# Kernel tuning notes

Hardware: AMD Instinct MI355X
Metric: run time of the kernel (lower is better)

Reference implementation:

```python
import jax, jax.numpy as jnp
import numpy as np

C = 64
K = 16
DEPTH = 4            # int(sqrt(K))
N_NODES = K - 1      # 15 internal nodes per subspace tree
D = 512              # input feature dim, D // C = 8 per subspace
M = 512              # output dim (LUT rows)
N = 16384            # number of input rows


def _make_selection_matrix(C, depth=DEPTH):
    # row i within a subspace selects the transformed dim used at tree level of node i
    lvl = [0, 1, 1, 2, 2, 2, 2, 3, 3, 3, 3, 3, 3, 3, 3]
    S = np.zeros((C * N_NODES, C * depth), np.float32)
    for c in range(C):
        for i in range(N_NODES):
            S[c * N_NODES + i, c * depth + lvl[i]] = 1.0
    return S


def _make_bit_matrix(C, K=K):
    # per-subspace (K, K-1) matrix: leaf k gets +/-1 on the 4 nodes along its root-to-leaf path
    Bm = np.zeros((K, N_NODES), np.float32)
    for k in range(K):
        node = 0
        for l in range(DEPTH):
            bit = (k >> (DEPTH - 1 - l)) & 1
            Bm[k, node] = 1.0 if bit else -1.0
            node = 2 * node + 1 + bit  # children of node i are 2i+1 (left) and 2i+2 (right)
    Bfull = np.zeros((C * K, C * N_NODES), np.float32)
    for c in range(C):
        Bfull[c * K:(c + 1) * K, c * N_NODES:(c + 1) * N_NODES] = Bm
    return Bfull


def setup_inputs() -> dict:
    key = jax.random.key(0)
    k1, k2, k3, k4 = jax.random.split(key, 4)
    I = jax.random.normal(k1, (N, D), dtype=jnp.float32)
    A = jax.random.normal(k2, (C, D // C, DEPTH), dtype=jnp.float32) * (1.0 / np.sqrt(D // C))
    T = jax.random.normal(k3, (C * N_NODES,), dtype=jnp.float32) * 0.1
    L = jax.random.normal(k4, (M, C, K), dtype=jnp.float32)
    S = jnp.asarray(_make_selection_matrix(C))
    B = jnp.asarray(_make_bit_matrix(C))
    return {"I": I, "A": A, "T": T, "L": L, "S": S, "B": B}


def reference(I, A, T, L, S, B):
    C_, sub, depth = A.shape
    Kq = L.shape[-1]
    n = I.shape[0]
    # block-diagonal per-subspace projection: (n, D) -> (n, C*depth)
    Ir = I.T.reshape(C_, sub, n)                      # (C, sub, n)
    xt = jnp.einsum('csn,csd->cdn', Ir, A)            # (C, depth, n)
    xt = xt.reshape(C_ * depth, n)                    # (C*depth, n)
    # tree encoding: per-node activations, tanh relaxation, leaf scores
    h = S @ xt - T[:, None]                           # (C*15, n)
    b = (B @ jnp.tanh(h)).reshape(C_, Kq, n)          # (C, K, n)
    # straight-through hard one-hot encoding with softmax backward
    E_soft = jax.nn.softmax(b, axis=1)
    E_hard = jax.nn.one_hot(jnp.argmax(b, axis=1), Kq, axis=1, dtype=b.dtype)
    E = E_hard + E_soft - jax.lax.stop_gradient(E_soft)  # (C, K, n)
    # LUT decode: out[n, m] = sum_c L[m, c, enc(n, c)]
    out = jnp.einsum('mck,ckn->nm', L, E)
    return out
```

## Files before the change

kernel.cpp:

```cpp
#include <hip/hip_runtime.h>
#include <hip/hip_fp16.h>
#include <math.h>

#define CC 64
#define KK 16
#define NNODES 15
#define DD 512
#define MM 512
#define NN 16384

typedef _Float16 half8 __attribute__((ext_vector_type(8)));
typedef float f32x4 __attribute__((ext_vector_type(4)));
typedef unsigned long long u64;

__device__ __forceinline__ float xla_tanhf(float x) {
    const float kMax = 7.90531110763549805f;
    bool tiny = fabsf(x) < 0.0004f;
    float xc = fminf(fmaxf(x, -kMax), kMax);
    float x2 = __fmul_rn(xc, xc);
    float p = __fmaf_rn(x2, -2.76076847742355e-16f, 2.00018790482477e-13f);
    p = __fmaf_rn(x2, p, -8.60467152213735e-11f);
    p = __fmaf_rn(x2, p, 5.12229709037114e-08f);
    p = __fmaf_rn(x2, p, 1.48572235717979e-05f);
    p = __fmaf_rn(x2, p, 6.37261928875436e-04f);
    p = __fmaf_rn(x2, p, 4.89352455891786e-03f);
    p = __fmul_rn(xc, p);
    float q = __fmaf_rn(x2, 1.19825839466702e-06f, 1.18534705686654e-04f);
    q = __fmaf_rn(x2, q, 2.26843463243900e-03f);
    q = __fmaf_rn(x2, q, 4.89352518554385e-03f);
    return tiny ? x : __fdiv_rn(p, q);
}

__global__ __launch_bounds__(256) void pack_bfrag(const float* __restrict__ L,
                                                  uint4* __restrict__ Bpk) {
    const int t    = blockIdx.x * 256 + threadIdx.x;
    const int lane = t & 63;
    const int mtg  = (t >> 6) & 31;
    const int ks   = t >> 11;
    const int kbase = ks * 32 + ((lane >> 4) << 3);
    const int c     = kbase >> 4;
    const int slot0 = kbase & 15;
    const int m     = (mtg << 4) + (lane & 15);

    const float* src = L + ((size_t)m * CC + c) * KK + slot0;
    float4 v0 = ((const float4*)src)[0];
    float4 v1 = ((const float4*)src)[1];
    union { half8 h; uint4 u; } pk;
    pk.h[0] = (_Float16)v0.x; pk.h[1] = (_Float16)v0.y;
    pk.h[2] = (_Float16)v0.z; pk.h[3] = (_Float16)v0.w;
    pk.h[4] = (_Float16)v1.x; pk.h[5] = (_Float16)v1.y;
    pk.h[6] = (_Float16)v1.z; pk.h[7] = (_Float16)v1.w;
    Bpk[t] = pk.u;
}

__global__ __launch_bounds__(256, 2) void fused_mfma(const float* __restrict__ I,
                                                     const float* __restrict__ A,
                                                     const float* __restrict__ T,
                                                     const uint4* __restrict__ Bpk,
                                                     float* __restrict__ out) {
    __shared__ float sA[32 * 64];
    __shared__ float sT[CC * NNODES];
    __shared__ unsigned char sCodes[CC * 68];

    const int tid = threadIdx.x;
    for (int i = tid; i < CC * 32; i += 256) sA[(i & 31) * 64 + (i >> 5)] = A[i];
    for (int i = tid; i < CC * NNODES; i += 256) sT[i] = T[i];
    __syncthreads();

    const int w    = tid >> 6;
    const int lane = tid & 63;
    const int n0 = (blockIdx.x >> 1) * 64;
    const int m0 = (blockIdx.x & 1) * 256 + w * 64;

    {
        const int c = lane;
        const int lvl[NNODES] = {0, 1, 1, 2, 2, 2, 2, 3, 3, 3, 3, 3, 3, 3, 3};
#pragma unroll 2
        for (int rr = 0; rr < 16; ++rr) {
            const int rl = (rr << 2) + w;
            const float* Ij = I + (size_t)(n0 + rl) * DD + c * 8;
            float4 v0 = ((const float4*)Ij)[0];
            float4 v1 = ((const float4*)Ij)[1];
            float iv[8] = {v0.x, v0.y, v0.z, v0.w, v1.x, v1.y, v1.z, v1.w};

            float t[4] = {0.f, 0.f, 0.f, 0.f};
#pragma unroll
            for (int s = 0; s < 8; ++s) {
                float v = iv[s];
#pragma unroll
                for (int d = 0; d < 4; ++d)
                    t[d] = __fmaf_rn(v, sA[((s << 2) + d) * 64 + c], t[d]);
            }

            float th[NNODES];
#pragma unroll
            for (int i = 0; i < NNODES; ++i) {
                float h = __fsub_rn(t[lvl[i]], sT[c * NNODES + i]);
                th[i] = xla_tanhf(h);
            }

            int best = 0;
            float bestv = -3.0e38f;
#pragma unroll
            for (int k = 0; k < KK; ++k) {
                int node = 0;
                float s = 0.f;
#pragma unroll
                for (int l = 0; l < 4; ++l) {
                    int bit = (k >> (3 - l)) & 1;
                    s = __fadd_rn(s, bit ? th[node] : -th[node]);
                    node = 2 * node + 1 + bit;
                }
                if (s > bestv) { bestv = s; best = k; }
            }
            sCodes[c * 68 + rl] = (unsigned char)best;
        }
    }
    __syncthreads();

    const int r15  = lane & 15;
    const int sb   = ((lane >> 4) & 1) << 3;
    const int chi  = lane >> 5;
    const int mtg0 = m0 >> 4;

    f32x4 acc[4][4];
#pragma unroll
    for (int nt = 0; nt < 4; ++nt)
#pragma unroll
        for (int mt = 0; mt < 4; ++mt)
            acc[nt][mt] = (f32x4){0.f, 0.f, 0.f, 0.f};

    const uint4* Bp = Bpk + (size_t)mtg0 * 64 + lane;

    uint4 bA[4], bB[4];
#pragma unroll
    for (int mt = 0; mt < 4; ++mt) bA[mt] = Bp[mt * 64];

    for (int ks = 0; ks < 32; ks += 2) {
#pragma unroll
        for (int mt = 0; mt < 4; ++mt) bB[mt] = Bp[((ks + 1) * 32 + mt) * 64];

        half8 a0[4];
        {
            const int c0 = (ks << 1) + chi;
#pragma unroll
            for (int nt = 0; nt < 4; ++nt) {
                unsigned ud = (unsigned)((int)sCodes[c0 * 68 + (nt << 4) + r15] - sb);
                unsigned ud2 = ud - 4u;
                u64 lo = (ud  < 4u) ? (0x3C00ull << ((ud  & 3u) << 4)) : 0ull;
                u64 hi = (ud2 < 4u) ? (0x3C00ull << ((ud2 & 3u) << 4)) : 0ull;
                union { u64 q[2]; half8 h; } uu; uu.q[0] = lo; uu.q[1] = hi;
                a0[nt] = uu.h;
            }
        }
#pragma unroll
        for (int nt = 0; nt < 4; ++nt)
#pragma unroll
            for (int mt = 0; mt < 4; ++mt) {
                union { uint4 u; half8 h; } bb; bb.u = bA[mt];
                acc[nt][mt] = __builtin_amdgcn_mfma_f32_16x16x32_f16(a0[nt], bb.h, acc[nt][mt], 0, 0, 0);
            }

        if (ks + 2 < 32) {
#pragma unroll
            for (int mt = 0; mt < 4; ++mt) bA[mt] = Bp[((ks + 2) * 32 + mt) * 64];
        }

        half8 a1[4];
        {
            const int c1 = ((ks + 1) << 1) + chi;
#pragma unroll
            for (int nt = 0; nt < 4; ++nt) {
                unsigned ud = (unsigned)((int)sCodes[c1 * 68 + (nt << 4) + r15] - sb);
                unsigned ud2 = ud - 4u;
                u64 lo = (ud  < 4u) ? (0x3C00ull << ((ud  & 3u) << 4)) : 0ull;
                u64 hi = (ud2 < 4u) ? (0x3C00ull << ((ud2 & 3u) << 4)) : 0ull;
                union { u64 q[2]; half8 h; } uu; uu.q[0] = lo; uu.q[1] = hi;
                a1[nt] = uu.h;
            }
        }
#pragma unroll
        for (int nt = 0; nt < 4; ++nt)
#pragma unroll
            for (int mt = 0; mt < 4; ++mt) {
                union { uint4 u; half8 h; } bb; bb.u = bB[mt];
                acc[nt][mt] = __builtin_amdgcn_mfma_f32_16x16x32_f16(a1[nt], bb.h, acc[nt][mt], 0, 0, 0);
            }
    }

    const int rbase = (lane >> 4) << 2;
#pragma unroll
    for (int nt = 0; nt < 4; ++nt) {
#pragma unroll
        for (int r = 0; r < 4; ++r) {
            float* o = out + (size_t)(n0 + (nt << 4) + rbase + r) * MM + m0 + r15;
#pragma unroll
            for (int mt = 0; mt < 4; ++mt)
                o[mt << 4] = acc[nt][mt][r];
        }
    }
}

extern "C" void kernel_launch(void* const* d_in, const int* in_sizes, int n_in,
                              void* d_out, int out_size, void* d_ws, size_t ws_size,
                              hipStream_t stream) {
    const float* I = (const float*)d_in[0];
    const float* A = (const float*)d_in[1];
    const float* T = (const float*)d_in[2];
    const float* L = (const float*)d_in[3];

    uint4* Bpk = (uint4*)d_ws;
    float* out = (float*)d_out;

    hipLaunchKernelGGL(pack_bfrag, dim3(256), dim3(256), 0, stream, L, Bpk);
    hipLaunchKernelGGL(fused_mfma, dim3(NN / 16 / 4 * 2), dim3(256), 0, stream, I, A, T, Bpk, out);
}
```

Before: 130.2 us.

## Use 512-thread blocks with narrower per-wave M tiles and packed code words

Doubles the block to 8 waves, with each wave covering 32 output columns instead of 64. This halves the accumulator registers per wave and splits the encoding work over 8 waves instead of 4. Codes are stored in shared memory as packed 4-byte words, one per (row, subspace) group, so each MFMA step needs one LDS read per k-step instead of four byte reads. B-fragment and code loads are software-prefetched one iteration ahead. The goal is higher occupancy and latency hiding, at the cost of a smaller N×M tile per wave, which may raise the global B-fragment traffic per FLOP.

```diff
diff --git a/kernel.cpp b/kernel.cpp
--- a/kernel.cpp
+++ b/kernel.cpp
@@ -53,31 +53,31 @@
     Bpk[t] = pk.u;
 }
 
-__global__ __launch_bounds__(256, 2) void fused_mfma(const float* __restrict__ I,
+__global__ __launch_bounds__(512, 4) void fused_mfma(const float* __restrict__ I,
                                                      const float* __restrict__ A,
                                                      const float* __restrict__ T,
                                                      const uint4* __restrict__ Bpk,
                                                      float* __restrict__ out) {
     __shared__ float sA[32 * 64];
     __shared__ float sT[CC * NNODES];
-    __shared__ unsigned char sCodes[CC * 68];
+    __shared__ unsigned sCodes[16 * 68];
 
     const int tid = threadIdx.x;
-    for (int i = tid; i < CC * 32; i += 256) sA[(i & 31) * 64 + (i >> 5)] = A[i];
-    for (int i = tid; i < CC * NNODES; i += 256) sT[i] = T[i];
+    for (int i = tid; i < CC * 32; i += 512) sA[(i & 31) * 64 + (i >> 5)] = A[i];
+    for (int i = tid; i < CC * NNODES; i += 512) sT[i] = T[i];
     __syncthreads();
 
     const int w    = tid >> 6;
     const int lane = tid & 63;
     const int n0 = (blockIdx.x >> 1) * 64;
-    const int m0 = (blockIdx.x & 1) * 256 + w * 64;
+    const int m0 = (blockIdx.x & 1) * 256 + w * 32;
 
     {
         const int c = lane;
         const int lvl[NNODES] = {0, 1, 1, 2, 2, 2, 2, 3, 3, 3, 3, 3, 3, 3, 3};
 #pragma unroll 2
-        for (int rr = 0; rr < 16; ++rr) {
-            const int rl = (rr << 2) + w;
+        for (int rr = 0; rr < 8; ++rr) {
+            const int rl = (rr << 3) + w;
             const float* Ij = I + (size_t)(n0 + rl) * DD + c * 8;
             float4 v0 = ((const float4*)Ij)[0];
             float4 v1 = ((const float4*)Ij)[1];
@@ -113,7 +113,7 @@
                 }
                 if (s > bestv) { bestv = s; best = k; }
             }
-            sCodes[c * 68 + rl] = (unsigned char)best;
+            ((unsigned char*)&sCodes[(rl & 15) * 68 + c])[rl >> 4] = (unsigned char)best;
         }
     }
     __syncthreads();
@@ -123,69 +123,76 @@
     const int chi  = lane >> 5;
     const int mtg0 = m0 >> 4;
 
-    f32x4 acc[4][4];
-#pragma unroll
-    for (int nt = 0; nt < 4; ++nt)
-#pragma unroll
-        for (int mt = 0; mt < 4; ++mt)
-            acc[nt][mt] = (f32x4){0.f, 0.f, 0.f, 0.f};
+    f32x4 acc[4][2];
+#pragma unroll
+    for (int nt = 0; nt < 4; ++nt) {
+        acc[nt][0] = (f32x4){0.f, 0.f, 0.f, 0.f};
+        acc[nt][1] = (f32x4){0.f, 0.f, 0.f, 0.f};
+    }
 
     const uint4* Bp = Bpk + (size_t)mtg0 * 64 + lane;
-
-    uint4 bA[4], bB[4];
-#pragma unroll
-    for (int mt = 0; mt < 4; ++mt) bA[mt] = Bp[mt * 64];
+    const unsigned* codeRow = sCodes + r15 * 68;
+
+    uint4 b0m0 = Bp[(0 * 32 + 0) * 64], b0m1 = Bp[(0 * 32 + 1) * 64];
+    uint4 b1m0 = Bp[(1 * 32 + 0) * 64], b1m1 = Bp[(1 * 32 + 1) * 64];
+    unsigned cw0 = codeRow[0 + chi];
+    unsigned cw1 = codeRow[2 + chi];
 
     for (int ks = 0; ks < 32; ks += 2) {
-#pragma unroll
-        for (int mt = 0; mt < 4; ++mt) bB[mt] = Bp[((ks + 1) * 32 + mt) * 64];
-
-        half8 a0[4];
+        uint4 n0m0, n0m1, n1m0, n1m1;
+        unsigned nw0, nw1;
+        const bool more = (ks + 2) < 32;
+        if (more) {
+            n0m0 = Bp[((ks + 2) * 32 + 0) * 64];
+            n0m1 = Bp[((ks + 2) * 32 + 1) * 64];
+            n1m0 = Bp[((ks + 3) * 32 + 0) * 64];
+            n1m1 = Bp[((ks + 3) * 32 + 1) * 64];
+            nw0 = codeRow[(ks + 2) * 2 + chi];
+            nw1 = codeRow[(ks + 3) * 2 + chi];
+        }
+
         {
-            const int c0 = (ks << 1) + chi;
-#pragma unroll
-            for (int nt = 0; nt < 4; ++nt) {
-                unsigned ud = (unsigned)((int)sCodes[c0 * 68 + (nt << 4) + r15] - sb);
+            half8 a[4];
+#pragma unroll
+            for (int nt = 0; nt < 4; ++nt) {
+                unsigned ud  = ((cw0 >> (nt << 3)) & 255u) - (unsigned)sb;
                 unsigned ud2 = ud - 4u;
                 u64 lo = (ud  < 4u) ? (0x3C00ull << ((ud  & 3u) << 4)) : 0ull;
                 u64 hi = (ud2 < 4u) ? (0x3C00ull << ((ud2 & 3u) << 4)) : 0ull;
                 union { u64 q[2]; half8 h; } uu; uu.q[0] = lo; uu.q[1] = hi;
-                a0[nt] = uu.h;
-            }
-        }
-#pragma unroll
-        for (int nt = 0; nt < 4; ++nt)
-#pragma unroll
-            for (int mt = 0; mt < 4; ++mt) {
-                union { uint4 u; half8 h; } bb; bb.u = bA[mt];
-                acc[nt][mt] = __builtin_amdgcn_mfma_f32_16x16x32_f16(a0[nt], bb.h, acc[nt][mt], 0, 0, 0);
-            }
-
-        if (ks + 2 < 32) {
-#pragma unroll
-            for (int mt = 0; mt < 4; ++mt) bA[mt] = Bp[((ks + 2) * 32 + mt) * 64];
-        }
-
-        half8 a1[4];
+                a[nt] = uu.h;
+            }
+            union { uint4 u; half8 h; } bb0, bb1; bb0.u = b0m0; bb1.u = b0m1;
+#pragma unroll
+            for (int nt = 0; nt < 4; ++nt) {
+                acc[nt][0] = __builtin_amdgcn_mfma_f32_16x16x32_f16(a[nt], bb0.h, acc[nt][0], 0, 0, 0);
+                acc[nt][1] = __builtin_amdgcn_mfma_f32_16x16x32_f16(a[nt], bb1.h, acc[nt][1], 0, 0, 0);
+            }
+        }
+
         {
-            const int c1 = ((ks + 1) << 1) + chi;
-#pragma unroll
-            for (int nt = 0; nt < 4; ++nt) {
-                unsigned ud = (unsigned)((int)sCodes[c1 * 68 + (nt << 4) + r15] - sb);
+            half8 a[4];
+#pragma unroll
+            for (int nt = 0; nt < 4; ++nt) {
+                unsigned ud  = ((cw1 >> (nt << 3)) & 255u) - (unsigned)sb;
                 unsigned ud2 = ud - 4u;
                 u64 lo = (ud  < 4u) ? (0x3C00ull << ((ud  & 3u) << 4)) : 0ull;
                 u64 hi = (ud2 < 4u) ? (0x3C00ull << ((ud2 & 3u) << 4)) : 0ull;
                 union { u64 q[2]; half8 h; } uu; uu.q[0] = lo; uu.q[1] = hi;
-                a1[nt] = uu.h;
-            }
-        }
-#pragma unroll
-        for (int nt = 0; nt < 4; ++nt)
-#pragma unroll
-            for (int mt = 0; mt < 4; ++mt) {
-                union { uint4 u; half8 h; } bb; bb.u = bB[mt];
-                acc[nt][mt] = __builtin_amdgcn_mfma_f32_16x16x32_f16(a1[nt], bb.h, acc[nt][mt], 0, 0, 0);
-            }
+                a[nt] = uu.h;
+            }
+            union { uint4 u; half8 h; } bb0, bb1; bb0.u = b1m0; bb1.u = b1m1;
+#pragma unroll
+            for (int nt = 0; nt < 4; ++nt) {
+                acc[nt][0] = __builtin_amdgcn_mfma_f32_16x16x32_f16(a[nt], bb0.h, acc[nt][0], 0, 0, 0);
+                acc[nt][1] = __builtin_amdgcn_mfma_f32_16x16x32_f16(a[nt], bb1.h, acc[nt][1], 0, 0, 0);
+            }
+        }
+
+        if (more) {
+            b0m0 = n0m0; b0m1 = n0m1; b1m0 = n1m0; b1m1 = n1m1;
+            cw0 = nw0; cw1 = nw1;
+        }
     }
 
     const int rbase = (lane >> 4) << 2;
@@ -194,9 +201,8 @@
 #pragma unroll
         for (int r = 0; r < 4; ++r) {
             float* o = out + (size_t)(n0 + (nt << 4) + rbase + r) * MM + m0 + r15;
-#pragma unroll
-            for (int mt = 0; mt < 4; ++mt)
-                o[mt << 4] = acc[nt][mt][r];
+            o[0]  = acc[nt][0][r];
+            o[16] = acc[nt][1][r];
         }
     }
 }
@@ -213,5 +219,5 @@
     float* out = (float*)d_out;
 
     hipLaunchKernelGGL(pack_bfrag, dim3(256), dim3(256), 0, stream, L, Bpk);
-    hipLaunchKernelGGL(fused_mfma, dim3(NN / 16 / 4 * 2), dim3(256), 0, stream, I, A, T, Bpk, out);
-}
+    hipLaunchKernelGGL(fused_mfma, dim3(512), dim3(512), 0, stream, I, A, T, Bpk, out);
+}
```

Result: slower. 182.2 us (+40.0%).

## Use 1024-thread blocks covering full M per 64-row tile to avoid duplicate encoding

Applied to the files above, without the earlier changes.

Each block now handles 64 rows and all 512 output columns with 16 waves, instead of two blocks per row tile that each recomputed the tree encoding. Every code is computed once, and codes are packed four per 32-bit word in shared memory so one read supplies the A fragment. Each wave computes a 16x128 tile with 8 accumulators instead of 64x64. The trade is less reuse of each loaded B fragment (one A tile per B), so the load on B fragments from global/L2 roughly quadruples, and 1024-thread blocks cap occupancy at one block per CU.

```diff
diff --git a/kernel.cpp b/kernel.cpp
--- a/kernel.cpp
+++ b/kernel.cpp
@@ -53,31 +53,31 @@
     Bpk[t] = pk.u;
 }
 
-__global__ __launch_bounds__(256, 2) void fused_mfma(const float* __restrict__ I,
-                                                     const float* __restrict__ A,
-                                                     const float* __restrict__ T,
-                                                     const uint4* __restrict__ Bpk,
-                                                     float* __restrict__ out) {
+__global__ __launch_bounds__(1024, 1) void fused_mfma(const float* __restrict__ I,
+                                                      const float* __restrict__ A,
+                                                      const float* __restrict__ T,
+                                                      const uint4* __restrict__ Bpk,
+                                                      float* __restrict__ out) {
     __shared__ float sA[32 * 64];
     __shared__ float sT[CC * NNODES];
-    __shared__ unsigned char sCodes[CC * 68];
+    __shared__ unsigned sCodes[16 * 68];
 
     const int tid = threadIdx.x;
-    for (int i = tid; i < CC * 32; i += 256) sA[(i & 31) * 64 + (i >> 5)] = A[i];
-    for (int i = tid; i < CC * NNODES; i += 256) sT[i] = T[i];
+    for (int i = tid; i < CC * 32; i += 1024) sA[(i & 31) * 64 + (i >> 5)] = A[i];
+    for (int i = tid; i < CC * NNODES; i += 1024) sT[i] = T[i];
     __syncthreads();
 
     const int w    = tid >> 6;
     const int lane = tid & 63;
-    const int n0 = (blockIdx.x >> 1) * 64;
-    const int m0 = (blockIdx.x & 1) * 256 + w * 64;
+    const int n0   = blockIdx.x * 64;
 
     {
         const int c = lane;
         const int lvl[NNODES] = {0, 1, 1, 2, 2, 2, 2, 3, 3, 3, 3, 3, 3, 3, 3};
+        unsigned codeWord = 0;
 #pragma unroll 2
-        for (int rr = 0; rr < 16; ++rr) {
-            const int rl = (rr << 2) + w;
+        for (int rr = 0; rr < 4; ++rr) {
+            const int rl = (rr << 4) + w;
             const float* Ij = I + (size_t)(n0 + rl) * DD + c * 8;
             float4 v0 = ((const float4*)Ij)[0];
             float4 v1 = ((const float4*)Ij)[1];
@@ -113,90 +113,76 @@
                 }
                 if (s > bestv) { bestv = s; best = k; }
             }
-            sCodes[c * 68 + rl] = (unsigned char)best;
-        }
+            codeWord |= ((unsigned)best) << (rr << 3);
+        }
+        sCodes[w * 68 + c] = codeWord;
     }
     __syncthreads();
 
+    const int wn   = w & 3;
+    const int wm   = w >> 2;
     const int r15  = lane & 15;
     const int sb   = ((lane >> 4) & 1) << 3;
     const int chi  = lane >> 5;
-    const int mtg0 = m0 >> 4;
-
-    f32x4 acc[4][4];
-#pragma unroll
-    for (int nt = 0; nt < 4; ++nt)
-#pragma unroll
-        for (int mt = 0; mt < 4; ++mt)
-            acc[nt][mt] = (f32x4){0.f, 0.f, 0.f, 0.f};
-
-    const uint4* Bp = Bpk + (size_t)mtg0 * 64 + lane;
-
-    uint4 bA[4], bB[4];
-#pragma unroll
-    for (int mt = 0; mt < 4; ++mt) bA[mt] = Bp[mt * 64];
+
+    f32x4 acc[8];
+#pragma unroll
+    for (int mt = 0; mt < 8; ++mt) acc[mt] = (f32x4){0.f, 0.f, 0.f, 0.f};
+
+    const uint4* Bp = Bpk + (size_t)(wm * 8) * 64 + lane;
+    const unsigned* codeRow = sCodes + r15 * 68;
+    const int wnsh = wn << 3;
+
+    uint4 bX[8], bY[8];
+#pragma unroll
+    for (int mt = 0; mt < 8; ++mt) bX[mt] = Bp[mt * 64];
+    unsigned cwA = codeRow[chi];
+    unsigned cwB;
 
     for (int ks = 0; ks < 32; ks += 2) {
 #pragma unroll
-        for (int mt = 0; mt < 4; ++mt) bB[mt] = Bp[((ks + 1) * 32 + mt) * 64];
-
-        half8 a0[4];
+        for (int mt = 0; mt < 8; ++mt) bY[mt] = Bp[((ks + 1) * 32 + mt) * 64];
+        cwB = codeRow[(ks + 1) * 2 + chi];
+
         {
-            const int c0 = (ks << 1) + chi;
-#pragma unroll
-            for (int nt = 0; nt < 4; ++nt) {
-                unsigned ud = (unsigned)((int)sCodes[c0 * 68 + (nt << 4) + r15] - sb);
-                unsigned ud2 = ud - 4u;
-                u64 lo = (ud  < 4u) ? (0x3C00ull << ((ud  & 3u) << 4)) : 0ull;
-                u64 hi = (ud2 < 4u) ? (0x3C00ull << ((ud2 & 3u) << 4)) : 0ull;
-                union { u64 q[2]; half8 h; } uu; uu.q[0] = lo; uu.q[1] = hi;
-                a0[nt] = uu.h;
-            }
-        }
-#pragma unroll
-        for (int nt = 0; nt < 4; ++nt)
-#pragma unroll
-            for (int mt = 0; mt < 4; ++mt) {
-                union { uint4 u; half8 h; } bb; bb.u = bA[mt];
-                acc[nt][mt] = __builtin_amdgcn_mfma_f32_16x16x32_f16(a0[nt], bb.h, acc[nt][mt], 0, 0, 0);
-            }
+            unsigned ud  = ((cwA >> wnsh) & 255u) - (unsigned)sb;
+            unsigned ud2 = ud - 4u;
+            u64 lo = (ud  < 4u) ? (0x3C00ull << ((ud  & 3u) << 4)) : 0ull;
+            u64 hi = (ud2 < 4u) ? (0x3C00ull << ((ud2 & 3u) << 4)) : 0ull;
+            union { u64 q[2]; half8 h; } uu; uu.q[0] = lo; uu.q[1] = hi;
+#pragma unroll
+            for (int mt = 0; mt < 8; ++mt) {
+                union { uint4 u; half8 h; } bb; bb.u = bX[mt];
+                acc[mt] = __builtin_amdgcn_mfma_f32_16x16x32_f16(uu.h, bb.h, acc[mt], 0, 0, 0);
+            }
+        }
 
         if (ks + 2 < 32) {
 #pragma unroll
-            for (int mt = 0; mt < 4; ++mt) bA[mt] = Bp[((ks + 2) * 32 + mt) * 64];
-        }
-
-        half8 a1[4];
+            for (int mt = 0; mt < 8; ++mt) bX[mt] = Bp[((ks + 2) * 32 + mt) * 64];
+            cwA = codeRow[(ks + 2) * 2 + chi];
+        }
+
         {
-            const int c1 = ((ks + 1) << 1) + chi;
-#pragma unroll
-            for (int nt = 0; nt < 4; ++nt) {
-                unsigned ud = (unsigned)((int)sCodes[c1 * 68 + (nt << 4) + r15] - sb);
-                unsigned ud2 = ud - 4u;
-                u64 lo = (ud  < 4u) ? (0x3C00ull << ((ud  & 3u) << 4)) : 0ull;
-                u64 hi = (ud2 < 4u) ? (0x3C00ull << ((ud2 & 3u) << 4)) : 0ull;
-                union { u64 q[2]; half8 h; } uu; uu.q[0] = lo; uu.q[1] = hi;
-                a1[nt] = uu.h;
-            }
-        }
-#pragma unroll
-        for (int nt = 0; nt < 4; ++nt)
-#pragma unroll
-            for (int mt = 0; mt < 4; ++mt) {
-                union { uint4 u; half8 h; } bb; bb.u = bB[mt];
-                acc[nt][mt] = __builtin_amdgcn_mfma_f32_16x16x32_f16(a1[nt], bb.h, acc[nt][mt], 0, 0, 0);
-            }
+            unsigned ud  = ((cwB >> wnsh) & 255u) - (unsigned)sb;
+            unsigned ud2 = ud - 4u;
+            u64 lo = (ud  < 4u) ? (0x3C00ull << ((ud  & 3u) << 4)) : 0ull;
+            u64 hi = (ud2 < 4u) ? (0x3C00ull << ((ud2 & 3u) << 4)) : 0ull;
+            union { u64 q[2]; half8 h; } uu; uu.q[0] = lo; uu.q[1] = hi;
+#pragma unroll
+            for (int mt = 0; mt < 8; ++mt) {
+                union { uint4 u; half8 h; } bb; bb.u = bY[mt];
+                acc[mt] = __builtin_amdgcn_mfma_f32_16x16x32_f16(uu.h, bb.h, acc[mt], 0, 0, 0);
+            }
+        }
     }
 
     const int rbase = (lane >> 4) << 2;
 #pragma unroll
-    for (int nt = 0; nt < 4; ++nt) {
+    for (int mt = 0; mt < 8; ++mt) {
 #pragma unroll
         for (int r = 0; r < 4; ++r) {
-            float* o = out + (size_t)(n0 + (nt << 4) + rbase + r) * MM + m0 + r15;
-#pragma unroll
-            for (int mt = 0; mt < 4; ++mt)
-                o[mt << 4] = acc[nt][mt][r];
+            out[(size_t)(n0 + (wn << 4) + rbase + r) * MM + (wm << 7) + (mt << 4) + r15] = acc[mt][r];
         }
     }
 }
@@ -213,5 +199,5 @@
     float* out = (float*)d_out;
 
     hipLaunchKernelGGL(pack_bfrag, dim3(256), dim3(256), 0, stream, L, Bpk);
-    hipLaunchKernelGGL(fused_mfma, dim3(NN / 16 / 4 * 2), dim3(256), 0, stream, I, A, T, Bpk, out);
-}
+    hipLaunchKernelGGL(fused_mfma, dim3(NN / 64), dim3(1024), 0, stream, I, A, T, Bpk, out);
+}
```

After: 133.0 us. 1.02x slower.
